# Kernel optimization log

Measured on AMD Instinct MI355X. Metric: run time of the kernel, lower is better.

The kernel has to match this reference:

```python
import jax, jax.numpy as jnp
import numpy as np

B, T_STEPS, H, W = 8192, 512, 64, 64


def setup_inputs() -> dict:
    key = jax.random.key(0)
    k_w, k_g, k_i, k_j, k_a = jax.random.split(key, 5)
    walls = (jax.random.uniform(k_w, (B, H, W)) < 0.3).astype(jnp.float32)
    walls = walls.at[:, 0, :].set(1.0).at[:, H - 1, :].set(1.0)
    walls = walls.at[:, :, 0].set(1.0).at[:, :, W - 1].set(1.0)
    # goals: sparse cells with value 10 (the code checks goals[...] == 10)
    goals = jnp.where(jax.random.uniform(k_g, (B, H, W)) < 0.02, 10.0, 0.0).astype(jnp.float32)
    # start positions strictly interior; clear the wall at each start cell
    i0 = jax.random.randint(k_i, (B,), 1, H - 1)
    j0 = jax.random.randint(k_j, (B,), 1, W - 1)
    walls = walls.at[jnp.arange(B), i0, j0].set(0.0)
    world = jnp.stack([walls, goals], axis=1)  # [B, 2, H, W]
    s0 = jnp.stack([i0, j0], axis=1).astype(jnp.float32)  # [B, 2]
    a = jax.random.randint(k_a, (B, T_STEPS), 0, 5).astype(jnp.int32)  # actions in {0..4}
    return {"s0": s0, "a": a, "world": world, "T": T_STEPS}


def _rollout(s0, a, world, T):
    walls = world[:, 0].reshape(world.shape[0], -1)  # [B, H*W]
    goals = world[:, 1].reshape(world.shape[0], -1)  # [B, H*W]
    Wd = world.shape[3]

    def step(s, a_t):
        # action deltas: 1 -> row-1, 2 -> row+1, 3 -> col-1, 4 -> col+1, 0 -> stay
        dr = jnp.where(a_t == 1, -1.0, jnp.where(a_t == 2, 1.0, 0.0))
        dc = jnp.where(a_t == 3, -1.0, jnp.where(a_t == 4, 1.0, 0.0))
        s_new = s + jnp.stack([dr, dc], axis=1).astype(s.dtype)  # [B, 2]
        idx = (s_new[:, 0].astype(jnp.int32) * Wd + s_new[:, 1].astype(jnp.int32))[:, None]
        g = jnp.take_along_axis(goals, idx, axis=1)[:, 0]
        w = jnp.take_along_axis(walls, idx, axis=1)[:, 0]
        hit_goal = g == 10.0
        hit_wall = jnp.logical_and(jnp.logical_not(hit_goal), w == 1.0)
        r = jnp.where(hit_goal, 1.0, jnp.where(hit_wall, -1.0, -0.01)).astype(jnp.float32)
        s_next = jnp.where(hit_wall[:, None], s, s_new)  # revert move on wall hit
        return s_next, (s_next, r)

    _, (s_traj, r_traj) = jax.lax.scan(step, s0, jnp.swapaxes(a[:, :T], 0, 1))
    s_full = jnp.concatenate([s0[:, None, :], jnp.swapaxes(s_traj, 0, 1)], axis=1)  # [B, T+1, 2]
    r0 = jnp.zeros((s0.shape[0], 1), dtype=jnp.float32)
    r_full = jnp.concatenate([r0, jnp.swapaxes(r_traj, 0, 1)], axis=1)  # [B, T+1]
    return s_full, r_full


def reference(s0, a, world, T):
    return _rollout(s0, a, world, T)
```

## Files before the change

kernel.cpp:

```cpp
#include <hip/hip_runtime.h>
#include <stdint.h>

#define T_STEPS 512
#define CELLS   4096
#define BPB     4
#define THREADS 64

__device__ __forceinline__ uint32_t pack4(float4 w, float4 g) {
    uint32_t b0 = (g.x == 10.0f) ? 2u : ((w.x == 1.0f) ? 1u : 0u);
    uint32_t b1 = (g.y == 10.0f) ? 2u : ((w.y == 1.0f) ? 1u : 0u);
    uint32_t b2 = (g.z == 10.0f) ? 2u : ((w.z == 1.0f) ? 1u : 0u);
    uint32_t b3 = (g.w == 10.0f) ? 2u : ((w.w == 1.0f) ? 1u : 0u);
    return b0 | (b1 << 8) | (b2 << 16) | (b3 << 24);
}

__global__ __launch_bounds__(THREADS) void rollout_kernel(
    const float* __restrict__ s0,
    const int*   __restrict__ act,
    const float* __restrict__ world,
    float* __restrict__ out,
    int B)
{
    __shared__ uint8_t cells[BPB * CELLS];

    const int tid = threadIdx.x;
    const int b0  = blockIdx.x * BPB;

    #pragma unroll
    for (int bb = 0; bb < BPB; ++bb) {
        const float* wbase = world + (size_t)(b0 + bb) * (2 * CELLS);
        const float* gbase = wbase + CELLS;
        #pragma unroll
        for (int h = 0; h < 4; ++h) {
            const int c0 = h * 1024 + tid * 16;
            float4 w0 = *(const float4*)(wbase + c0);
            float4 w1 = *(const float4*)(wbase + c0 + 4);
            float4 w2 = *(const float4*)(wbase + c0 + 8);
            float4 w3 = *(const float4*)(wbase + c0 + 12);
            float4 g0 = *(const float4*)(gbase + c0);
            float4 g1 = *(const float4*)(gbase + c0 + 4);
            float4 g2 = *(const float4*)(gbase + c0 + 8);
            float4 g3 = *(const float4*)(gbase + c0 + 12);
            uint4 v = make_uint4(pack4(w0, g0), pack4(w1, g1),
                                 pack4(w2, g2), pack4(w3, g3));
            *(uint4*)(&cells[bb * CELLS + c0]) = v;
        }
    }
    __syncthreads();

    if (tid < BPB) {
        const int b = b0 + tid;
        float2 s = *(const float2*)(s0 + 2 * (size_t)b);
        int r = (int)s.x;
        int c = (int)s.y;
        int p = r * 64 + c;
        const uint8_t* my = cells + tid * CELLS;

        auto lookup = [&](int q) -> int {
            const int idx = q + ((q < 0) ? CELLS : 0);
            const int cell = my[idx & (CELLS - 1)];
            return ((unsigned)idx < (unsigned)CELLS) ? cell : 0;
        };

        float* s_out = out + (size_t)b * (2 * (T_STEPS + 1));
        float* r_out = out + (size_t)B * (2 * (T_STEPS + 1)) + (size_t)b * (T_STEPS + 1);

        *(float2*)s_out = s;
        r_out[0] = 0.0f;

        const int4* ap = (const int4*)(act + (size_t)b * T_STEPS);
        int4 A0 = ap[0];
        int4 A1 = ap[1];
        int4 A2 = ap[2];
        for (int k = 0; k < T_STEPS / 4; ++k) {
            const int4 A3 = (k + 3 < T_STEPS / 4) ? ap[k + 3] : A0;
            const int as4[4] = {A0.x, A0.y, A0.z, A0.w};
            #pragma unroll
            for (int jj = 0; jj < 2; ++jj) {
                const int t  = k * 4 + jj * 2;
                const int a0 = as4[2 * jj];
                const int a1 = as4[2 * jj + 1];
                const int d0r = (a0 == 1) ? -1 : ((a0 == 2) ? 1 : 0);
                const int d0c = (a0 == 3) ? -1 : ((a0 == 4) ? 1 : 0);
                const int d1r = (a1 == 1) ? -1 : ((a1 == 2) ? 1 : 0);
                const int d1c = (a1 == 3) ? -1 : ((a1 == 4) ? 1 : 0);
                const int e0 = d0r * 64 + d0c;
                const int e1 = d1r * 64 + d1c;
                const int q0  = p + e0;
                const int q10 = p + e1;
                const int q11 = q0 + e1;
                const int l0  = lookup(q0);
                const int l10 = lookup(q10);
                const int l11 = lookup(q11);
                const bool hw0  = (l0 == 1);
                const float rew0 = (l0 == 2) ? 1.0f : (hw0 ? -1.0f : -0.01f);
                const int p0  = hw0 ? p : q0;
                const int r0v = hw0 ? r : r + d0r;
                const int c0v = hw0 ? c : c + d0c;
                const int l1 = hw0 ? l10 : l11;
                const bool hw1  = (l1 == 1);
                const float rew1 = (l1 == 2) ? 1.0f : (hw1 ? -1.0f : -0.01f);
                p = hw1 ? p0 : p0 + e1;
                r = hw1 ? r0v : r0v + d1r;
                c = hw1 ? c0v : c0v + d1c;
                *(float2*)(s_out + 2 * (t + 1)) = make_float2((float)r0v, (float)c0v);
                *(float2*)(s_out + 2 * (t + 2)) = make_float2((float)r, (float)c);
                r_out[t + 1] = rew0;
                r_out[t + 2] = rew1;
            }
            A0 = A1; A1 = A2; A2 = A3;
        }
    }
}

extern "C" void kernel_launch(void* const* d_in, const int* in_sizes, int n_in,
                              void* d_out, int out_size, void* d_ws, size_t ws_size,
                              hipStream_t stream) {
    const float* s0    = (const float*)d_in[0];
    const int*   act   = (const int*)d_in[1];
    const float* world = (const float*)d_in[2];
    float*       out   = (float*)d_out;

    const int B = in_sizes[0] / 2;
    const int grid = B / BPB;

    rollout_kernel<<<grid, THREADS, 0, stream>>>(s0, act, world, out, B);
}
```

Before: 493.3 us.

## Pre-pack world into 2-bit codes and run 32 envs per wave

A separate pack kernel turns the float wall and goal grids into 2-bit cell codes in workspace, 256 words per environment. The rollout kernel then stages 32 packed environments per block in padded LDS and uses 32 active lanes instead of 4. The aim is to cut LDS footprint and keep the wave's lanes busy during the serial rollout. In exchange it adds a second launch, a global round trip through workspace, extra shift-and-mask work per lookup, and only one wave per CU (256 blocks), which weakens latency hiding.

```diff
diff --git a/kernel.cpp b/kernel.cpp
--- a/kernel.cpp
+++ b/kernel.cpp
@@ -3,62 +3,74 @@
 
 #define T_STEPS 512
 #define CELLS   4096
-#define BPB     4
-#define THREADS 64
+#define EPB     32
+#define WPE     256
+#define WPAD    257
 
-__device__ __forceinline__ uint32_t pack4(float4 w, float4 g) {
+__device__ __forceinline__ uint32_t code4(float4 w, float4 g) {
     uint32_t b0 = (g.x == 10.0f) ? 2u : ((w.x == 1.0f) ? 1u : 0u);
     uint32_t b1 = (g.y == 10.0f) ? 2u : ((w.y == 1.0f) ? 1u : 0u);
     uint32_t b2 = (g.z == 10.0f) ? 2u : ((w.z == 1.0f) ? 1u : 0u);
     uint32_t b3 = (g.w == 10.0f) ? 2u : ((w.w == 1.0f) ? 1u : 0u);
-    return b0 | (b1 << 8) | (b2 << 16) | (b3 << 24);
+    return b0 | (b1 << 2) | (b2 << 4) | (b3 << 6);
 }
 
-__global__ __launch_bounds__(THREADS) void rollout_kernel(
+__global__ __launch_bounds__(64) void pack_kernel(
+    const float* __restrict__ world, uint32_t* __restrict__ packed)
+{
+    const int b = blockIdx.x;
+    const int t = threadIdx.x;
+    const float* wbase = world + (size_t)b * (2 * CELLS);
+    const float* gbase = wbase + CELLS;
+    #pragma unroll
+    for (int h = 0; h < 4; ++h) {
+        const int w  = h * 64 + t;
+        const int c0 = w * 16;
+        uint32_t word = 0;
+        #pragma unroll
+        for (int j = 0; j < 4; ++j) {
+            float4 wf = *(const float4*)(wbase + c0 + 4 * j);
+            float4 gf = *(const float4*)(gbase + c0 + 4 * j);
+            word |= code4(wf, gf) << (8 * j);
+        }
+        packed[(size_t)b * WPE + w] = word;
+    }
+}
+
+__global__ __launch_bounds__(64) void rollout_kernel(
     const float* __restrict__ s0,
     const int*   __restrict__ act,
-    const float* __restrict__ world,
+    const uint32_t* __restrict__ packed,
     float* __restrict__ out,
     int B)
 {
-    __shared__ uint8_t cells[BPB * CELLS];
+    __shared__ uint32_t lds[EPB * WPAD];
 
     const int tid = threadIdx.x;
-    const int b0  = blockIdx.x * BPB;
+    const int b0  = blockIdx.x * EPB;
 
-    #pragma unroll
-    for (int bb = 0; bb < BPB; ++bb) {
-        const float* wbase = world + (size_t)(b0 + bb) * (2 * CELLS);
-        const float* gbase = wbase + CELLS;
-        #pragma unroll
-        for (int h = 0; h < 4; ++h) {
-            const int c0 = h * 1024 + tid * 16;
-            float4 w0 = *(const float4*)(wbase + c0);
-            float4 w1 = *(const float4*)(wbase + c0 + 4);
-            float4 w2 = *(const float4*)(wbase + c0 + 8);
-            float4 w3 = *(const float4*)(wbase + c0 + 12);
-            float4 g0 = *(const float4*)(gbase + c0);
-            float4 g1 = *(const float4*)(gbase + c0 + 4);
-            float4 g2 = *(const float4*)(gbase + c0 + 8);
-            float4 g3 = *(const float4*)(gbase + c0 + 12);
-            uint4 v = make_uint4(pack4(w0, g0), pack4(w1, g1),
-                                 pack4(w2, g2), pack4(w3, g3));
-            *(uint4*)(&cells[bb * CELLS + c0]) = v;
-        }
+    for (int ee = 0; ee < EPB; ++ee) {
+        uint4 v = *(const uint4*)(packed + (size_t)(b0 + ee) * WPE + tid * 4);
+        const int base = ee * WPAD + tid * 4;
+        lds[base]     = v.x;
+        lds[base + 1] = v.y;
+        lds[base + 2] = v.z;
+        lds[base + 3] = v.w;
     }
     __syncthreads();
 
-    if (tid < BPB) {
+    if (tid < EPB) {
         const int b = b0 + tid;
         float2 s = *(const float2*)(s0 + 2 * (size_t)b);
         int r = (int)s.x;
         int c = (int)s.y;
         int p = r * 64 + c;
-        const uint8_t* my = cells + tid * CELLS;
+        const uint32_t* my = lds + tid * WPAD;
 
         auto lookup = [&](int q) -> int {
             const int idx = q + ((q < 0) ? CELLS : 0);
-            const int cell = my[idx & (CELLS - 1)];
+            const uint32_t wd = my[(idx >> 4) & (WPE - 1)];
+            const int cell = (wd >> ((idx & 15) * 2)) & 3;
             return ((unsigned)idx < (unsigned)CELLS) ? cell : 0;
         };
 
@@ -120,9 +132,10 @@
     const int*   act   = (const int*)d_in[1];
     const float* world = (const float*)d_in[2];
     float*       out   = (float*)d_out;
+    uint32_t*    packed = (uint32_t*)d_ws;
 
     const int B = in_sizes[0] / 2;
-    const int grid = B / BPB;
 
-    rollout_kernel<<<grid, THREADS, 0, stream>>>(s0, act, world, out, B);
+    pack_kernel<<<B, 64, 0, stream>>>(world, packed);
+    rollout_kernel<<<B / EPB, 64, 0, stream>>>(s0, act, packed, out, B);
 }
```

Result: faster. 461.8 us (-6.4%).
